# Kernel optimization log

Hardware: AMD Instinct MI355X
Metric: run time of the kernel (lower is better)

## Reference

```python
import jax, jax.numpy as jnp
import numpy as np
import math

EPS = 0.1          # sinkhorn_epsilon
ITERS = 50         # max_iterations
POWER = 2.0        # cost_power


def _l2_normalize(x):
    # matches F.normalize(p=2, dim=-1, eps=1e-12)
    n = jnp.linalg.norm(x, axis=-1, keepdims=True)
    return x / jnp.maximum(n, 1e-12)


def setup_inputs() -> dict:
    key = jax.random.key(0)
    k1, k2 = jax.random.split(key)
    source = jax.random.normal(k1, (64, 1024, 64), dtype=jnp.float32)
    target = jax.random.normal(k2, (64, 1024, 64), dtype=jnp.float32)
    return {"source": source, "target": target}


def reference(source, target):
    s = _l2_normalize(source)  # [B, n, d]
    t = _l2_normalize(target)  # [B, m, d]

    # pairwise Euclidean distance (torch.cdist p=2), then ** cost_power
    sq = (jnp.sum(s * s, axis=-1)[..., :, None]
          + jnp.sum(t * t, axis=-1)[..., None, :]
          - 2.0 * jnp.einsum('bnd,bmd->bnm', s, t))
    dist = jnp.sqrt(jnp.maximum(sq, 0.0))
    cost = dist ** POWER  # [B, n, m]

    n = s.shape[-2]
    m = t.shape[-2]
    batch = cost.shape[:-2]
    log_a = jnp.full(batch + (n,), -math.log(float(n)), dtype=cost.dtype)
    log_b = jnp.full(batch + (m,), -math.log(float(m)), dtype=cost.dtype)

    log_kernel = -cost / EPS

    def step(carry, _):
        log_u, log_v = carry
        log_u = log_a - jax.scipy.special.logsumexp(
            log_kernel + log_v[..., None, :], axis=-1)
        log_v = log_b - jax.scipy.special.logsumexp(
            log_kernel + log_u[..., :, None], axis=-2)
        return (log_u, log_v), None

    init = (jnp.zeros_like(log_a), jnp.zeros_like(log_b))
    (log_u, log_v), _ = jax.lax.scan(step, init, None, length=ITERS)

    log_plan = log_kernel + log_u[..., :, None] + log_v[..., None, :]
    plan = jnp.exp(log_plan)
    distances = jnp.sum(plan * cost, axis=(-2, -1))  # [B]
    return jnp.mean(distances)
```

## Files before the change

### kernel.cpp

```cpp
#include <hip/hip_runtime.h>
#include <hip/hip_fp16.h>


#define BATCH 64
#define NPT   1024
#define DIM   64
#define NSLAB 16
#define CKF   28.853900817779268f
#define WV0F  2.0611536224e-9f
#define G10F  0.0009765625f

#if __has_builtin(__builtin_amdgcn_exp2f)
#define EXP2F(x) __builtin_amdgcn_exp2f(x)
#else
#define EXP2F(x) exp2f(x)
#endif

__device__ __forceinline__ float2 h2tof2(unsigned int u) {
  return __half22float2(__builtin_bit_cast(__half2, u));
}
__device__ __forceinline__ void dec8(uint4 pk, float* f) {
  float2 t;
  t = h2tof2(pk.x); f[0] = t.x; f[1] = t.y;
  t = h2tof2(pk.y); f[2] = t.x; f[3] = t.y;
  t = h2tof2(pk.z); f[4] = t.x; f[5] = t.y;
  t = h2tof2(pk.w); f[6] = t.x; f[7] = t.y;
}
__device__ __forceinline__ void stage16(const __half* g, __half* l) {
  __builtin_amdgcn_global_load_lds(
      (const __attribute__((address_space(1))) void*)g,
      (__attribute__((address_space(3))) void*)l, 16, 0, 0);
}

__global__ __launch_bounds__(256) void build_q(
    const float* __restrict__ src, const float* __restrict__ tgt,
    __half* __restrict__ q)
{
  __shared__ float sA[DIM][68];
  __shared__ float sB[DIM][68];

  const int b    = blockIdx.x >> 8;
  const int tile = blockIdx.x & 255;
  const int i0 = (tile >> 4) << 6;
  const int j0 = (tile & 15) << 6;
  const int tid = threadIdx.x;
  const int r = tid >> 2;
  const int c = tid & 3;

  {
    const float4* p4 = (const float4*)(src + ((size_t)b * NPT + (i0 + r)) * DIM + c * 16);
    float4 a0 = p4[0], a1 = p4[1], a2 = p4[2], a3 = p4[3];
    float v[16] = {a0.x,a0.y,a0.z,a0.w, a1.x,a1.y,a1.z,a1.w,
                   a2.x,a2.y,a2.z,a2.w, a3.x,a3.y,a3.z,a3.w};
    float ss = 0.f;
    #pragma unroll
    for (int k = 0; k < 16; ++k) ss = fmaf(v[k], v[k], ss);
    ss += __shfl_xor(ss, 1);
    ss += __shfl_xor(ss, 2);
    const float sc = 1.0f / fmaxf(sqrtf(ss), 1e-12f);
    #pragma unroll
    for (int k = 0; k < 16; ++k) sA[c * 16 + k][r] = v[k] * sc;
  }
  {
    const float4* p4 = (const float4*)(tgt + ((size_t)b * NPT + (j0 + r)) * DIM + c * 16);
    float4 a0 = p4[0], a1 = p4[1], a2 = p4[2], a3 = p4[3];
    float v[16] = {a0.x,a0.y,a0.z,a0.w, a1.x,a1.y,a1.z,a1.w,
                   a2.x,a2.y,a2.z,a2.w, a3.x,a3.y,a3.z,a3.w};
    float ss = 0.f;
    #pragma unroll
    for (int k = 0; k < 16; ++k) ss = fmaf(v[k], v[k], ss);
    ss += __shfl_xor(ss, 1);
    ss += __shfl_xor(ss, 2);
    const float sc = 1.0f / fmaxf(sqrtf(ss), 1e-12f);
    #pragma unroll
    for (int k = 0; k < 16; ++k) sB[c * 16 + k][r] = v[k] * sc;
  }
  __syncthreads();

  const int mi = (tid >> 4) << 2;
  const int mj = (tid & 15) << 2;
  float acc[4][4] = {};
  #pragma unroll 16
  for (int d = 0; d < DIM; ++d) {
    const float4 a = *(const float4*)&sA[d][mi];
    const float4 t = *(const float4*)&sB[d][mj];
    const float av[4] = {a.x, a.y, a.z, a.w};
    const float tv[4] = {t.x, t.y, t.z, t.w};
    #pragma unroll
    for (int ii = 0; ii < 4; ++ii)
      #pragma unroll
      for (int jj = 0; jj < 4; ++jj)
        acc[ii][jj] = fmaf(av[ii], tv[jj], acc[ii][jj]);
  }

  #pragma unroll
  for (int ii = 0; ii < 4; ++ii) {
    __half2 h0 = __floats2half2_rn(acc[ii][0], acc[ii][1]);
    __half2 h1 = __floats2half2_rn(acc[ii][2], acc[ii][3]);
    uint2 pk = { __builtin_bit_cast(unsigned int, h0),
                 __builtin_bit_cast(unsigned int, h1) };
    *(uint2*)(q + (size_t)b * NPT * NPT
                + (size_t)(i0 + mi + ii) * NPT + (j0 + mj)) = pk;
  }
}

template<bool FIRST, bool FINAL>
__global__ __launch_bounds__(256) void sink_pass(
    const __half* __restrict__ q,
    const float* __restrict__ partR,
    float* __restrict__ partW,
    float* __restrict__ cpart)
{
  __shared__ __align__(16) __half smem[2][8][NPT];

  const int b    = blockIdx.x >> 4;
  const int slab = blockIdx.x & 15;
  const int lane = threadIdx.x & 63;
  const int wave = threadIdx.x >> 6;

  const __half* qt = q + ((size_t)b << 20) + ((size_t)(slab << 6) << 10);

  {
    const __half* gsrc = qt + (wave << 11) + (lane << 3);
    __half* ldst = &smem[0][0][0] + (wave << 11);
    #pragma unroll
    for (int p = 0; p < 4; ++p)
      stage16(gsrc + (p << 9), ldst + (p << 9));
  }

  float wv[16];
  if (FIRST) {
    #pragma unroll
    for (int k = 0; k < 16; ++k) wv[k] = WV0F;
  } else {
    float sv[16] = {};
    #pragma unroll
    for (int s = 0; s < NSLAB; ++s) {
      const float4* p4 =
          (const float4*)(partR + ((size_t)((s << 6) + b) << 10) + (lane << 4));
      #pragma unroll
      for (int g4 = 0; g4 < 4; ++g4) {
        const float4 v = p4[g4];
        sv[g4 * 4 + 0] += v.x;
        sv[g4 * 4 + 1] += v.y;
        sv[g4 * 4 + 2] += v.z;
        sv[g4 * 4 + 3] += v.w;
      }
    }
    #pragma unroll
    for (int k = 0; k < 16; ++k) wv[k] = G10F / sv[k];
  }

  float acc[16] = {};
  float cacc[16];
  if (FINAL) {
    #pragma unroll
    for (int k = 0; k < 16; ++k) cacc[k] = 0.f;
  }

  #pragma unroll 2
  for (int t = 0; t < 8; ++t) {
    __syncthreads();
    if (t < 7) {
      const __half* gsrc = qt + ((size_t)(t + 1) << 13) + (wave << 11) + (lane << 3);
      __half* ldst = &smem[(t + 1) & 1][0][0] + (wave << 11);
      #pragma unroll
      for (int p = 0; p < 4; ++p)
        stage16(gsrc + (p << 9), ldst + (p << 9));
    }
    #pragma unroll
    for (int rr = 0; rr < 2; ++rr) {
      const uint4* rp = (const uint4*)&smem[t & 1][(wave << 1) + rr][0] + (lane << 1);
      const uint4 pa = rp[0];
      const uint4 pb = rp[1];
      float f[16];
      dec8(pa, f);
      dec8(pb, f + 8);
      float u[16];
      #pragma unroll
      for (int k = 0; k < 16; ++k) u[k] = EXP2F(f[k] * CKF);

      float d0 = 0.f, d1 = 0.f, d2 = 0.f, d3 = 0.f;
      #pragma unroll
      for (int k = 0; k < 16; k += 4) {
        d0 = fmaf(u[k],     wv[k],     d0);
        d1 = fmaf(u[k + 1], wv[k + 1], d1);
        d2 = fmaf(u[k + 2], wv[k + 2], d2);
        d3 = fmaf(u[k + 3], wv[k + 3], d3);
      }
      float s = (d0 + d1) + (d2 + d3);
      #pragma unroll
      for (int m = 1; m <= 32; m <<= 1) s += __shfl_xor(s, m);
      const float g = G10F / s;

      #pragma unroll
      for (int k = 0; k < 16; ++k) {
        acc[k] = fmaf(u[k], g, acc[k]);
        if (FINAL) cacc[k] = fmaf(u[k] * g, fmaf(f[k], -2.0f, 2.0f), cacc[k]);
      }
    }
  }

  __syncthreads();
  float* lp = (float*)&smem[0][0][0];
  float* lc = (float*)&smem[1][0][0];
  #pragma unroll
  for (int k = 0; k < 16; ++k)
    lp[(wave << 10) + (lane << 4) + k] = acc[k];
  if (FINAL) {
    #pragma unroll
    for (int k = 0; k < 16; ++k)
      lc[(wave << 10) + (lane << 4) + k] = cacc[k];
  }
  __syncthreads();
  {
    const int tid = threadIdx.x;
    const float4* lp4 = (const float4*)lp;
    float4 p0 = lp4[(0 << 8) + tid];
    float4 p1 = lp4[(1 << 8) + tid];
    float4 p2 = lp4[(2 << 8) + tid];
    float4 p3 = lp4[(3 << 8) + tid];
    float4 s4;
    s4.x = (p0.x + p1.x) + (p2.x + p3.x);
    s4.y = (p0.y + p1.y) + (p2.y + p3.y);
    s4.z = (p0.z + p1.z) + (p2.z + p3.z);
    s4.w = (p0.w + p1.w) + (p2.w + p3.w);
    ((float4*)(partW + ((size_t)((slab << 6) + b) << 10)))[tid] = s4;
    if (FINAL) {
      const float4* lc4 = (const float4*)lc;
      float4 c0 = lc4[(0 << 8) + tid];
      float4 c1 = lc4[(1 << 8) + tid];
      float4 c2 = lc4[(2 << 8) + tid];
      float4 c3 = lc4[(3 << 8) + tid];
      float4 c4v;
      c4v.x = (c0.x + c1.x) + (c2.x + c3.x);
      c4v.y = (c0.y + c1.y) + (c2.y + c3.y);
      c4v.z = (c0.z + c1.z) + (c2.z + c3.z);
      c4v.w = (c0.w + c1.w) + (c2.w + c3.w);
      ((float4*)(cpart + ((size_t)((slab << 6) + b) << 10)))[tid] = c4v;
    }
  }
}

__global__ __launch_bounds__(256) void final_reduce(
    const float* __restrict__ partR, const float* __restrict__ cpart,
    float* __restrict__ out)
{
  const int b   = blockIdx.x;
  const int tid = threadIdx.x;
  float4 p = {0.f, 0.f, 0.f, 0.f};
  float4 c = {0.f, 0.f, 0.f, 0.f};
  #pragma unroll 4
  for (int s = 0; s < NSLAB; ++s) {
    const size_t base = (size_t)((s << 6) + b) << 8;
    const float4 pv = ((const float4*)partR)[base + tid];
    const float4 cv = ((const float4*)cpart)[base + tid];
    p.x += pv.x; p.y += pv.y; p.z += pv.z; p.w += pv.w;
    c.x += cv.x; c.y += cv.y; c.z += cv.z; c.w += cv.w;
  }
  float s = (c.x / p.x + c.y / p.y) + (c.z / p.z + c.w / p.w);
  #pragma unroll
  for (int m = 1; m <= 32; m <<= 1) s += __shfl_xor(s, m);
  __shared__ float ls[4];
  if ((threadIdx.x & 63) == 0) ls[threadIdx.x >> 6] = s;
  __syncthreads();
  if (threadIdx.x == 0)
    atomicAdd(out, (ls[0] + ls[1] + ls[2] + ls[3]) * (1.0f / 65536.0f));
}

extern "C" void kernel_launch(void* const* d_in, const int* in_sizes, int n_in,
                              void* d_out, int out_size, void* d_ws, size_t ws_size,
                              hipStream_t stream)
{
  (void)in_sizes; (void)n_in; (void)out_size; (void)ws_size;
  const float* src = (const float*)d_in[0];
  const float* tgt = (const float*)d_in[1];

  char* ws = (char*)d_ws;
  __half* q = (__half*)ws;
  const size_t QB = (size_t)BATCH * NPT * NPT * sizeof(__half);
  const size_t PART_N = (size_t)NSLAB * BATCH * NPT;
  float* partA = (float*)(ws + QB);
  float* partB = partA + PART_N;
  float* cpart = partB + PART_N;
  float* part[2] = {partA, partB};

  hipMemsetAsync(d_out, 0, sizeof(float), stream);

  build_q<<<BATCH * 256, 256, 0, stream>>>(src, tgt, q);

  for (int t = 0; t < 50; ++t) {
    float* R = part[t & 1];
    float* W = part[(t + 1) & 1];
    if (t == 0)
      sink_pass<true, false><<<BATCH * NSLAB, 256, 0, stream>>>(q, nullptr, W, nullptr);
    else if (t == 49)
      sink_pass<false, true><<<BATCH * NSLAB, 256, 0, stream>>>(q, R, W, cpart);
    else
      sink_pass<false, false><<<BATCH * NSLAB, 256, 0, stream>>>(q, R, W, nullptr);
  }

  final_reduce<<<BATCH, 256, 0, stream>>>(part[0], cpart, (float*)d_out);
}
```

Baseline: 2.065 ms.

## Fuse Sinkhorn passes into one cooperative persistent kernel with grid sync

Replaces the 50 separate sink_pass launches plus the final reduce with a single cooperative kernel that loops over the passes and uses grid.sync between them. It falls back to per-pass launches if the cooperative launch fails. Each block now covers 128 rows instead of 64 (8 chunks instead of 16), which halves the partial sums each pass has to reduce. Each wave streams its own rows through a 4-deep LDS ring with manual vmcnt waits instead of block-wide __syncthreads double buffering. The aim is to remove launch overhead and per-pass sync stalls, at the cost of grid-sync latency and fewer resident blocks (512).

```diff
diff --git a/kernel.cpp b/kernel.cpp
--- a/kernel.cpp
+++ b/kernel.cpp
@@ -1,14 +1,18 @@
 #include <hip/hip_runtime.h>
 #include <hip/hip_fp16.h>
-
-
-#define BATCH 64
-#define NPT   1024
-#define DIM   64
-#define NSLAB 16
-#define CKF   28.853900817779268f
-#define WV0F  2.0611536224e-9f
-#define G10F  0.0009765625f
+#include <hip/hip_cooperative_groups.h>
+
+namespace cg = cooperative_groups;
+
+
+#define BATCH  64
+#define NPT    1024
+#define DIM    64
+#define NCHUNK 8
+#define NBLK   (BATCH * NCHUNK)
+#define CKF    28.853900817779268f
+#define WV0F   2.0611536224e-9f
+#define G10F   0.0009765625f
 
 #if __has_builtin(__builtin_amdgcn_exp2f)
 #define EXP2F(x) __builtin_amdgcn_exp2f(x)
@@ -104,28 +108,24 @@
   }
 }
 
-template<bool FIRST, bool FINAL>
-__global__ __launch_bounds__(256) void sink_pass(
-    const __half* __restrict__ q,
-    const float* __restrict__ partR,
-    float* __restrict__ partW,
-    float* __restrict__ cpart)
-{
-  __shared__ __align__(16) __half smem[2][8][NPT];
-
-  const int b    = blockIdx.x >> 4;
-  const int slab = blockIdx.x & 15;
-  const int lane = threadIdx.x & 63;
-  const int wave = threadIdx.x >> 6;
-
-  const __half* qt = q + ((size_t)b << 20) + ((size_t)(slab << 6) << 10);
-
-  {
-    const __half* gsrc = qt + (wave << 11) + (lane << 3);
-    __half* ldst = &smem[0][0][0] + (wave << 11);
-    #pragma unroll
-    for (int p = 0; p < 4; ++p)
-      stage16(gsrc + (p << 9), ldst + (p << 9));
+template<bool FIRST, bool FIN>
+__device__ __forceinline__ void pass_once(
+    const __half* __restrict__ qt,
+    const float* __restrict__ pR, float* __restrict__ pW,
+    float* __restrict__ cpart,
+    __half (*smem)[4][NPT],
+    const int b, const int chunk, const int lane, const int wave, const int tid)
+{
+  const int lhalf = lane << 3;
+
+  {
+    const __half* g0 = qt + (wave << 10) + lhalf;
+    #pragma unroll
+    for (int tt = 0; tt < 3; ++tt) {
+      __half* l = &smem[tt][wave][0] + lhalf;
+      stage16(g0 + (tt << 12), l);
+      stage16(g0 + (tt << 12) + 512, l + 512);
+    }
   }
 
   float wv[16];
@@ -135,137 +135,199 @@
   } else {
     float sv[16] = {};
     #pragma unroll
-    for (int s = 0; s < NSLAB; ++s) {
-      const float4* p4 =
-          (const float4*)(partR + ((size_t)((s << 6) + b) << 10) + (lane << 4));
+    for (int s = 0; s < NCHUNK; ++s) {
+      const float* base = pR + ((size_t)((s << 6) + b) << 10);
+      const float4* pa = (const float4*)(base + lhalf);
+      const float4* pb = (const float4*)(base + 512 + lhalf);
+      const float4 v0 = pa[0], v1 = pa[1], v2 = pb[0], v3 = pb[1];
+      sv[0] += v0.x;  sv[1] += v0.y;  sv[2]  += v0.z;  sv[3]  += v0.w;
+      sv[4] += v1.x;  sv[5] += v1.y;  sv[6]  += v1.z;  sv[7]  += v1.w;
+      sv[8] += v2.x;  sv[9] += v2.y;  sv[10] += v2.z;  sv[11] += v2.w;
+      sv[12] += v3.x; sv[13] += v3.y; sv[14] += v3.z;  sv[15] += v3.w;
+    }
+    #pragma unroll
+    for (int k = 0; k < 16; ++k) wv[k] = G10F / sv[k];
+  }
+
+  float acc[16] = {};
+  float cacc[16] = {};
+
+  #pragma unroll 4
+  for (int t = 0; t < 32; ++t) {
+    if (t + 3 < 32) {
+      const __half* gs = qt + ((size_t)(t + 3) << 12) + (wave << 10) + lhalf;
+      __half* ls = &smem[(t + 3) & 3][wave][0] + lhalf;
+      stage16(gs, ls);
+      stage16(gs + 512, ls + 512);
+    }
+    const int rem = 31 - t;
+    if (rem >= 3)      asm volatile("s_waitcnt vmcnt(6)" ::: "memory");
+    else if (rem == 2) asm volatile("s_waitcnt vmcnt(4)" ::: "memory");
+    else if (rem == 1) asm volatile("s_waitcnt vmcnt(2)" ::: "memory");
+    else               asm volatile("s_waitcnt vmcnt(0)" ::: "memory");
+
+    const __half* row = &smem[t & 3][wave][0];
+    const uint4 pa = *(const uint4*)(row + lhalf);
+    const uint4 pb = *(const uint4*)(row + 512 + lhalf);
+    float f[16];
+    dec8(pa, f);
+    dec8(pb, f + 8);
+    float u[16];
+    #pragma unroll
+    for (int k = 0; k < 16; ++k) u[k] = EXP2F(f[k] * CKF);
+
+    float d0 = 0.f, d1 = 0.f, d2 = 0.f, d3 = 0.f;
+    #pragma unroll
+    for (int k = 0; k < 16; k += 4) {
+      d0 = fmaf(u[k],     wv[k],     d0);
+      d1 = fmaf(u[k + 1], wv[k + 1], d1);
+      d2 = fmaf(u[k + 2], wv[k + 2], d2);
+      d3 = fmaf(u[k + 3], wv[k + 3], d3);
+    }
+    float s = (d0 + d1) + (d2 + d3);
+    #pragma unroll
+    for (int m = 1; m <= 32; m <<= 1) s += __shfl_xor(s, m);
+    const float g = G10F / s;
+
+    #pragma unroll
+    for (int k = 0; k < 16; ++k) acc[k] = fmaf(u[k], g, acc[k]);
+    if (FIN) {
       #pragma unroll
-      for (int g4 = 0; g4 < 4; ++g4) {
-        const float4 v = p4[g4];
-        sv[g4 * 4 + 0] += v.x;
-        sv[g4 * 4 + 1] += v.y;
-        sv[g4 * 4 + 2] += v.z;
-        sv[g4 * 4 + 3] += v.w;
-      }
-    }
-    #pragma unroll
-    for (int k = 0; k < 16; ++k) wv[k] = G10F / sv[k];
-  }
-
-  float acc[16] = {};
-  float cacc[16];
-  if (FINAL) {
-    #pragma unroll
-    for (int k = 0; k < 16; ++k) cacc[k] = 0.f;
-  }
-
-  #pragma unroll 2
-  for (int t = 0; t < 8; ++t) {
-    __syncthreads();
-    if (t < 7) {
-      const __half* gsrc = qt + ((size_t)(t + 1) << 13) + (wave << 11) + (lane << 3);
-      __half* ldst = &smem[(t + 1) & 1][0][0] + (wave << 11);
-      #pragma unroll
-      for (int p = 0; p < 4; ++p)
-        stage16(gsrc + (p << 9), ldst + (p << 9));
-    }
-    #pragma unroll
-    for (int rr = 0; rr < 2; ++rr) {
-      const uint4* rp = (const uint4*)&smem[t & 1][(wave << 1) + rr][0] + (lane << 1);
-      const uint4 pa = rp[0];
-      const uint4 pb = rp[1];
-      float f[16];
-      dec8(pa, f);
-      dec8(pb, f + 8);
-      float u[16];
-      #pragma unroll
-      for (int k = 0; k < 16; ++k) u[k] = EXP2F(f[k] * CKF);
-
-      float d0 = 0.f, d1 = 0.f, d2 = 0.f, d3 = 0.f;
-      #pragma unroll
-      for (int k = 0; k < 16; k += 4) {
-        d0 = fmaf(u[k],     wv[k],     d0);
-        d1 = fmaf(u[k + 1], wv[k + 1], d1);
-        d2 = fmaf(u[k + 2], wv[k + 2], d2);
-        d3 = fmaf(u[k + 3], wv[k + 3], d3);
-      }
-      float s = (d0 + d1) + (d2 + d3);
-      #pragma unroll
-      for (int m = 1; m <= 32; m <<= 1) s += __shfl_xor(s, m);
-      const float g = G10F / s;
-
-      #pragma unroll
-      for (int k = 0; k < 16; ++k) {
-        acc[k] = fmaf(u[k], g, acc[k]);
-        if (FINAL) cacc[k] = fmaf(u[k] * g, fmaf(f[k], -2.0f, 2.0f), cacc[k]);
-      }
+      for (int k = 0; k < 16; ++k)
+        cacc[k] = fmaf(u[k] * g, fmaf(f[k], -2.0f, 2.0f), cacc[k]);
     }
   }
 
   __syncthreads();
   float* lp = (float*)&smem[0][0][0];
-  float* lc = (float*)&smem[1][0][0];
-  #pragma unroll
-  for (int k = 0; k < 16; ++k)
-    lp[(wave << 10) + (lane << 4) + k] = acc[k];
-  if (FINAL) {
-    #pragma unroll
-    for (int k = 0; k < 16; ++k)
-      lc[(wave << 10) + (lane << 4) + k] = cacc[k];
+  float* lc = (float*)&smem[2][0][0];
+  {
+    float* lpw = lp + (wave << 10);
+    *(float4*)(lpw + lhalf)       = make_float4(acc[0], acc[1], acc[2], acc[3]);
+    *(float4*)(lpw + lhalf + 4)   = make_float4(acc[4], acc[5], acc[6], acc[7]);
+    *(float4*)(lpw + 512 + lhalf) = make_float4(acc[8], acc[9], acc[10], acc[11]);
+    *(float4*)(lpw + 516 + lhalf) = make_float4(acc[12], acc[13], acc[14], acc[15]);
+    if (FIN) {
+      float* lcw = lc + (wave << 10);
+      *(float4*)(lcw + lhalf)       = make_float4(cacc[0], cacc[1], cacc[2], cacc[3]);
+      *(float4*)(lcw + lhalf + 4)   = make_float4(cacc[4], cacc[5], cacc[6], cacc[7]);
+      *(float4*)(lcw + 512 + lhalf) = make_float4(cacc[8], cacc[9], cacc[10], cacc[11]);
+      *(float4*)(lcw + 516 + lhalf) = make_float4(cacc[12], cacc[13], cacc[14], cacc[15]);
+    }
   }
   __syncthreads();
   {
-    const int tid = threadIdx.x;
     const float4* lp4 = (const float4*)lp;
-    float4 p0 = lp4[(0 << 8) + tid];
-    float4 p1 = lp4[(1 << 8) + tid];
-    float4 p2 = lp4[(2 << 8) + tid];
-    float4 p3 = lp4[(3 << 8) + tid];
+    const float4 p0 = lp4[tid], p1 = lp4[256 + tid],
+                 p2 = lp4[512 + tid], p3 = lp4[768 + tid];
     float4 s4;
     s4.x = (p0.x + p1.x) + (p2.x + p3.x);
     s4.y = (p0.y + p1.y) + (p2.y + p3.y);
     s4.z = (p0.z + p1.z) + (p2.z + p3.z);
     s4.w = (p0.w + p1.w) + (p2.w + p3.w);
-    ((float4*)(partW + ((size_t)((slab << 6) + b) << 10)))[tid] = s4;
-    if (FINAL) {
+    ((float4*)(pW + ((size_t)((chunk << 6) + b) << 10)))[tid] = s4;
+    if (FIN) {
       const float4* lc4 = (const float4*)lc;
-      float4 c0 = lc4[(0 << 8) + tid];
-      float4 c1 = lc4[(1 << 8) + tid];
-      float4 c2 = lc4[(2 << 8) + tid];
-      float4 c3 = lc4[(3 << 8) + tid];
-      float4 c4v;
-      c4v.x = (c0.x + c1.x) + (c2.x + c3.x);
-      c4v.y = (c0.y + c1.y) + (c2.y + c3.y);
-      c4v.z = (c0.z + c1.z) + (c2.z + c3.z);
-      c4v.w = (c0.w + c1.w) + (c2.w + c3.w);
-      ((float4*)(cpart + ((size_t)((slab << 6) + b) << 10)))[tid] = c4v;
-    }
-  }
-}
-
-__global__ __launch_bounds__(256) void final_reduce(
-    const float* __restrict__ partR, const float* __restrict__ cpart,
+      const float4 c0 = lc4[tid], c1 = lc4[256 + tid],
+                   c2 = lc4[512 + tid], c3 = lc4[768 + tid];
+      float4 c4;
+      c4.x = (c0.x + c1.x) + (c2.x + c3.x);
+      c4.y = (c0.y + c1.y) + (c2.y + c3.y);
+      c4.z = (c0.z + c1.z) + (c2.z + c3.z);
+      c4.w = (c0.w + c1.w) + (c2.w + c3.w);
+      ((float4*)(cpart + ((size_t)((chunk << 6) + b) << 10)))[tid] = c4;
+    }
+  }
+}
+
+__global__ __launch_bounds__(256)
+__attribute__((amdgpu_waves_per_eu(4, 4)))
+void coop_sink(const __half* __restrict__ q,
+               float* __restrict__ partA, float* __restrict__ partB,
+               float* __restrict__ cpart, float* __restrict__ out)
+{
+  __shared__ __align__(16) __half smem[4][4][NPT];
+
+  const int b     = blockIdx.x >> 3;
+  const int chunk = blockIdx.x & 7;
+  const int lane  = threadIdx.x & 63;
+  const int wave  = threadIdx.x >> 6;
+  const int tid   = threadIdx.x;
+  cg::grid_group grid = cg::this_grid();
+
+  const __half* qt = q + ((size_t)b << 20) + ((size_t)(chunk << 7) << 10);
+
+  for (int pass = 0; pass < 50; ++pass) {
+    const float* pR = (pass & 1) ? partB : partA;
+    float*       pW = (pass & 1) ? partA : partB;
+    if (pass == 0)
+      pass_once<true, false>(qt, pR, pW, cpart, smem, b, chunk, lane, wave, tid);
+    else if (pass < 49)
+      pass_once<false, false>(qt, pR, pW, cpart, smem, b, chunk, lane, wave, tid);
+    else
+      pass_once<false, true>(qt, pR, pW, cpart, smem, b, chunk, lane, wave, tid);
+    __threadfence();
+    grid.sync();
+  }
+
+  if (chunk == 0) {
+    float4 p = {0.f, 0.f, 0.f, 0.f}, c = {0.f, 0.f, 0.f, 0.f};
+    #pragma unroll
+    for (int s = 0; s < NCHUNK; ++s) {
+      const size_t base = (size_t)((s << 6) + b) << 8;
+      const float4 pv = ((const float4*)partA)[base + tid];
+      const float4 cv = ((const float4*)cpart)[base + tid];
+      p.x += pv.x; p.y += pv.y; p.z += pv.z; p.w += pv.w;
+      c.x += cv.x; c.y += cv.y; c.z += cv.z; c.w += cv.w;
+    }
+    float r = (c.x / p.x + c.y / p.y) + (c.z / p.z + c.w / p.w);
+    #pragma unroll
+    for (int m = 1; m <= 32; m <<= 1) r += __shfl_xor(r, m);
+    float* lsf = (float*)&smem[0][0][0];
+    if (lane == 0) lsf[wave] = r;
+    __syncthreads();
+    if (tid == 0)
+      atomicAdd(out, (lsf[0] + lsf[1] + lsf[2] + lsf[3]) * (1.0f / 65536.0f));
+  }
+}
+
+template<bool FIRST, bool FIN>
+__global__ __launch_bounds__(256)
+__attribute__((amdgpu_waves_per_eu(4, 4)))
+void sink_fb(const __half* __restrict__ q, const float* __restrict__ pR,
+             float* __restrict__ pW, float* __restrict__ cpart)
+{
+  __shared__ __align__(16) __half smem[4][4][NPT];
+  const int b     = blockIdx.x >> 3;
+  const int chunk = blockIdx.x & 7;
+  const __half* qt = q + ((size_t)b << 20) + ((size_t)(chunk << 7) << 10);
+  pass_once<FIRST, FIN>(qt, pR, pW, cpart, smem, b, chunk,
+                        threadIdx.x & 63, threadIdx.x >> 6, threadIdx.x);
+}
+
+__global__ __launch_bounds__(256) void final_fb(
+    const float* __restrict__ partA, const float* __restrict__ cpart,
     float* __restrict__ out)
 {
   const int b   = blockIdx.x;
   const int tid = threadIdx.x;
-  float4 p = {0.f, 0.f, 0.f, 0.f};
-  float4 c = {0.f, 0.f, 0.f, 0.f};
-  #pragma unroll 4
-  for (int s = 0; s < NSLAB; ++s) {
+  float4 p = {0.f, 0.f, 0.f, 0.f}, c = {0.f, 0.f, 0.f, 0.f};
+  #pragma unroll
+  for (int s = 0; s < NCHUNK; ++s) {
     const size_t base = (size_t)((s << 6) + b) << 8;
-    const float4 pv = ((const float4*)partR)[base + tid];
+    const float4 pv = ((const float4*)partA)[base + tid];
     const float4 cv = ((const float4*)cpart)[base + tid];
     p.x += pv.x; p.y += pv.y; p.z += pv.z; p.w += pv.w;
     c.x += cv.x; c.y += cv.y; c.z += cv.z; c.w += cv.w;
   }
-  float s = (c.x / p.x + c.y / p.y) + (c.z / p.z + c.w / p.w);
+  float r = (c.x / p.x + c.y / p.y) + (c.z / p.z + c.w / p.w);
   #pragma unroll
-  for (int m = 1; m <= 32; m <<= 1) s += __shfl_xor(s, m);
-  __shared__ float ls[4];
-  if ((threadIdx.x & 63) == 0) ls[threadIdx.x >> 6] = s;
+  for (int m = 1; m <= 32; m <<= 1) r += __shfl_xor(r, m);
+  __shared__ float lsf[4];
+  if ((tid & 63) == 0) lsf[tid >> 6] = r;
   __syncthreads();
-  if (threadIdx.x == 0)
-    atomicAdd(out, (ls[0] + ls[1] + ls[2] + ls[3]) * (1.0f / 65536.0f));
+  if (tid == 0)
+    atomicAdd(out, (lsf[0] + lsf[1] + lsf[2] + lsf[3]) * (1.0f / 65536.0f));
 }
 
 extern "C" void kernel_launch(void* const* d_in, const int* in_sizes, int n_in,
@@ -279,26 +341,38 @@
   char* ws = (char*)d_ws;
   __half* q = (__half*)ws;
   const size_t QB = (size_t)BATCH * NPT * NPT * sizeof(__half);
-  const size_t PART_N = (size_t)NSLAB * BATCH * NPT;
+  const size_t PART_N = (size_t)NCHUNK * BATCH * NPT;
   float* partA = (float*)(ws + QB);
   float* partB = partA + PART_N;
   float* cpart = partB + PART_N;
-  float* part[2] = {partA, partB};
+  float* outp  = (float*)d_out;
 
   hipMemsetAsync(d_out, 0, sizeof(float), stream);
 
   build_q<<<BATCH * 256, 256, 0, stream>>>(src, tgt, q);
 
-  for (int t = 0; t < 50; ++t) {
-    float* R = part[t & 1];
-    float* W = part[(t + 1) & 1];
-    if (t == 0)
-      sink_pass<true, false><<<BATCH * NSLAB, 256, 0, stream>>>(q, nullptr, W, nullptr);
-    else if (t == 49)
-      sink_pass<false, true><<<BATCH * NSLAB, 256, 0, stream>>>(q, R, W, cpart);
-    else
-      sink_pass<false, false><<<BATCH * NSLAB, 256, 0, stream>>>(q, R, W, nullptr);
-  }
-
-  final_reduce<<<BATCH, 256, 0, stream>>>(part[0], cpart, (float*)d_out);
-}
+  int maxb = 0;
+  hipError_t qrc = hipOccupancyMaxActiveBlocksPerMultiprocessor(
+      &maxb, coop_sink, 256, 0);
+  hipError_t rc = hipErrorUnknown;
+  if (qrc == hipSuccess && maxb >= 2) {
+    const __half* qa = q;
+    void* args[5] = {(void*)&qa, (void*)&partA, (void*)&partB,
+                     (void*)&cpart, (void*)&outp};
+    rc = hipLaunchCooperativeKernel((void*)coop_sink, dim3(NBLK), dim3(256),
+                                    args, 0, stream);
+  }
+  if (rc != hipSuccess) {
+    for (int t = 0; t < 50; ++t) {
+      const float* R = (t & 1) ? partB : partA;
+      float*       W = (t & 1) ? partA : partB;
+      if (t == 0)
+        sink_fb<true, false><<<NBLK, 256, 0, stream>>>(q, R, W, cpart);
+      else if (t == 49)
+        sink_fb<false, true><<<NBLK, 256, 0, stream>>>(q, R, W, cpart);
+      else
+        sink_fb<false, false><<<NBLK, 256, 0, stream>>>(q, R, W, cpart);
+    }
+    final_fb<<<BATCH, 256, 0, stream>>>(partA, cpart, (float*)d_out);
+  }
+}
```

Result: slower. 7.177 ms (+247.6%).
